# Performance work log

Hardware: AMD Instinct MI355X
Metric: run time of the kernel (lower is better)

The kernel has to match this reference:

```python
import jax, jax.numpy as jnp
import numpy as np
import math

B, T, D, S, V = 128, 32, 64, 32, 8192
MAX_REC = 8
PONDER = 0.01
TWO_PI = 2.0 * math.pi


def setup_inputs():
    key = jax.random.key(0)
    ks = jax.random.split(key, 12)
    sd = 1.0 / math.sqrt(D)
    g = lambda k, shape, s: jax.random.normal(k, shape, jnp.float32) * s
    return {
        "x_seq": jax.random.randint(ks[0], (B, T), 0, V),
        "encoder_emb": g(ks[1], (V, 2 * D), 0.02),
        "vq_emb": g(ks[2], (V, 2 * D), sd),
        "norm_rg": jnp.ones((D,), jnp.float32), "norm_rb": jnp.zeros((D,), jnp.float32),
        "norm_ig": jnp.ones((D,), jnp.float32), "norm_ib": jnp.zeros((D,), jnp.float32),
        "qkv_Wr": g(ks[3], (3, D, D), sd), "qkv_br": g(ks[4], (3, D), sd),
        "qkv_Wi": g(ks[5], (3, D, D), sd), "qkv_bi": g(ks[6], (3, D), sd),
        "gate_w": g(ks[7], (2 * D,), sd), "gate_b": jnp.zeros((), jnp.float32),
        "arb_W": g(ks[8], (3, 2 * D), sd), "arb_b": jnp.zeros((3,), jnp.float32),
        "dec_W": g(ks[9], (V, 2 * D), sd), "dec_b": jnp.zeros((V,), jnp.float32),
        "halt_bias": jnp.asarray(3.0, jnp.float32),
        "input_gate": jnp.asarray(0.0, jnp.float32),
    }


def _ln(x, g, b, eps=1e-5):
    mu = x.mean(-1, keepdims=True)
    var = ((x - mu) ** 2).mean(-1, keepdims=True)
    return (x - mu) * jax.lax.rsqrt(var + eps) * g + b


def _forward(x_seq, encoder_emb, vq_emb, norm_rg, norm_rb, norm_ig, norm_ib,
             qkv_Wr, qkv_br, qkv_Wi, qkv_bi, gate_w, gate_b, arb_W, arb_b,
             dec_W, dec_b, halt_bias, input_gate):
    sg = jax.lax.stop_gradient
    e_sq = (vq_emb ** 2).sum(-1)  # [V]
    alpha = jax.nn.sigmoid(input_gate)
    bias = jax.nn.softplus(halt_bias)

    def clin(xr, xi, Wr, br, Wi, bi):
        # torch ComplexLinear: real = fc_r(xr) - fc_i(xi); imag = fc_r(xi) + fc_i(xr)
        return (xr @ Wr.T + br) - (xi @ Wi.T + bi), (xi @ Wr.T + br) + (xr @ Wi.T + bi)

    def mem_write(gr, gi, mr, mi):
        flat = jnp.concatenate([gr, gi], -1)
        wg = jax.nn.sigmoid(flat @ gate_w + gate_b)[:, None, None]  # [B,1,1]
        shr, shi = jnp.roll(mr, 1, axis=1), jnp.roll(mi, 1, axis=1)
        hr = wg * gr[:, None, :] + (1.0 - wg) * shr[:, :1]
        hi = wg * gi[:, None, :] + (1.0 - wg) * shi[:, :1]
        return jnp.concatenate([hr, shr[:, 1:]], 1), jnp.concatenate([hi, shi[:, 1:]], 1)

    def time_step(carry, xt):
        gw_r, gw_i, mem_r, mem_i = carry
        x_r, x_i = xt
        gw_r = alpha * gw_r + (1.0 - alpha) * x_r
        gw_i = alpha * gw_i + (1.0 - alpha) * x_i
        active = jnp.ones((B,), jnp.float32)
        acc_vq = jnp.zeros((B,), jnp.float32)
        acc_ent = jnp.zeros((B,), jnp.float32)
        acc_pond = jnp.zeros((B,), jnp.float32)
        acc_ph = jnp.zeros((B,), jnp.float32)
        fin_idx = jnp.zeros((B,), jnp.int32)
        prev_ang = jnp.arctan2(gw_i, gw_r)
        for _ in range(MAX_REC):
            cr = _ln(gw_r, norm_rg, norm_rb)
            ci = _ln(gw_i, norm_ig, norm_ib)
            z_flat = jnp.concatenate([cr, ci], -1)  # [B,2D]
            # squared-euclidean scores; argmin identical to cdist argmin
            d2 = (z_flat ** 2).sum(-1, keepdims=True) - 2.0 * (z_flat @ vq_emb.T) + e_sq
            idx = jnp.argmin(d2, -1).astype(jnp.int32)
            z_q = vq_emb[idx]
            vq_loss = ((z_q - sg(z_flat)) ** 2).mean(-1) + 0.25 * ((sg(z_q) - z_flat) ** 2).mean(-1)
            z_st = z_flat + sg(z_q - z_flat)  # straight-through
            counts = jnp.zeros((V,), jnp.float32).at[idx].add(1.0) / B
            entropy = -(counts * jnp.log(counts + 1e-10)).sum()
            v_r, v_i = z_st[:, :D], z_st[:, D:]
            # Hermitian gating
            qr, qi = clin(cr, ci, qkv_Wr[0], qkv_br[0], qkv_Wi[0], qkv_bi[0])
            kr, ki = clin(cr, ci, qkv_Wr[1], qkv_br[1], qkv_Wi[1], qkv_bi[1])
            vr2, vi2 = clin(cr, ci, qkv_Wr[2], qkv_br[2], qkv_Wi[2], qkv_bi[2])
            gate = jax.nn.sigmoid((qr * kr + qi * ki).sum(-1, keepdims=True))
            g_r, g_i = vr2 * gate, vi2 * gate
            # memory read (Re<m, q> attention over slots)
            sim = jnp.einsum('bsd,bd->bs', mem_r, cr) + jnp.einsum('bsd,bd->bs', mem_i, ci)
            attn = jax.nn.softmax(sim, -1)
            m_r = jnp.einsum('bs,bsd->bd', attn, mem_r)
            m_i = jnp.einsum('bs,bsd->bd', attn, mem_i)
            gates = jax.nn.softmax(z_flat @ arb_W.T + arb_b, -1)  # [B,3]
            upd_r = gates[:, 0:1] * g_r + gates[:, 1:2] * m_r + gates[:, 2:3] * v_r
            upd_i = gates[:, 0:1] * g_i + gates[:, 1:2] * m_i + gates[:, 2:3] * v_i
            cand_r = 0.6 * cr + 0.4 * upd_r
            cand_i = 0.6 * ci + 0.4 * upd_i
            ang = jnp.arctan2(cand_i, cand_r)
            diff = jnp.abs(ang - prev_ang)
            diff = jnp.minimum(diff, TWO_PI - diff)
            acc_ph = acc_ph + active * diff.mean(-1)
            prev_ang = ang
            halt_prob = jax.nn.sigmoid(bias - vq_loss)
            should_stop = (halt_prob > 0.5).astype(jnp.float32)
            acc_pond = acc_pond + active * PONDER
            mflat = active > 0.5
            acc_vq = jnp.where(mflat, vq_loss, acc_vq)
            acc_ent = jnp.where(mflat, entropy, acc_ent)
            fin_idx = jnp.where(mflat, idx, fin_idx)
            am = mflat[:, None]
            gw_r = jnp.where(am, cand_r, gw_r)
            gw_i = jnp.where(am, cand_i, gw_i)
            active = active * (1.0 - should_stop)
        mem_r, mem_i = mem_write(gw_r, gw_i, mem_r, mem_i)
        stats_t = jnp.stack([acc_vq.mean(), acc_ent.mean(), acc_pond.mean(), acc_ph.mean()])
        return (gw_r, gw_i, mem_r, mem_i), (gw_r, gw_i, fin_idx, stats_t)

    emb = encoder_emb[x_seq]  # [B,T,2D]
    xr = jnp.transpose(emb[..., :D], (1, 0, 2))  # [T,B,D]
    xi = jnp.transpose(emb[..., D:], (1, 0, 2))
    init = (jnp.zeros((B, D), jnp.float32), jnp.zeros((B, D), jnp.float32),
            jnp.zeros((B, S, D), jnp.float32), jnp.zeros((B, S, D), jnp.float32))
    _, (out_r, out_i, idxs, stats) = jax.lax.scan(time_step, init, (xr, xi))
    out = jnp.concatenate([jnp.transpose(out_r, (1, 0, 2)),
                           jnp.transpose(out_i, (1, 0, 2))], -1)  # [B,T,2D]
    logits = out @ dec_W.T + dec_b  # [B,T,V]
    return logits, stats.sum(0) / T, jnp.transpose(idxs)  # [B,T]


def reference(x_seq, encoder_emb, vq_emb, norm_rg, norm_rb, norm_ig, norm_ib, qkv_Wr, qkv_br, qkv_Wi, qkv_bi, gate_w, gate_b, arb_W, arb_b, dec_W, dec_b, halt_bias, input_gate):
    return _forward(x_seq, encoder_emb, vq_emb, norm_rg, norm_rb, norm_ig, norm_ib,
                    qkv_Wr, qkv_br, qkv_Wi, qkv_bi, gate_w, gate_b, arb_W, arb_b,
                    dec_W, dec_b, halt_bias, input_gate)
```

## Files before the change

### kernel.cpp

```cpp
#include <hip/hip_runtime.h>
#include <math.h>

#define TT 32
#define MAXREC 8
#define NBLK 256
#define NTHR 1024

#define OFF_ZBUF   0u
#define OFF_KEYS   65536u
#define OFF_ZDONE  196608u
#define OFF_FINAL  198656u
#define OFF_OUTHB  200704u
#define OFF_RST    1249280u
#define OFF_DWB    1251328u

#define SENT 0x7FFFFFFFu
#define IDXM 0x1FFFu
#define LOGN 33554432u
#define TWO_PI_F 6.283185307179586f

typedef float f32x4 __attribute__((ext_vector_type(4)));
typedef short bf16x8 __attribute__((ext_vector_type(8)));
typedef unsigned long long u64;

__device__ __forceinline__ float wredsum(float v) {
#pragma unroll
  for (int m = 32; m > 0; m >>= 1) v += __shfl_xor(v, m);
  return v;
}

__device__ __forceinline__ u64 shflx64(u64 v, int m) {
  int lo = __shfl_xor((int)(unsigned)(v & 0xffffffffull), m);
  int hi = __shfl_xor((int)(unsigned)(v >> 32), m);
  return ((u64)(unsigned)hi << 32) | (unsigned)lo;
}

__device__ __forceinline__ u64 packkey(float d, unsigned c) {
  unsigned u = __float_as_uint(d);
  u = (u & 0x80000000u) ? ~u : (u | 0x80000000u);
  return ((u64)u << 32) | c;
}
__device__ __forceinline__ float unpackd2(u64 key) {
  unsigned hi = (unsigned)(key >> 32);
  unsigned orig = (hi & 0x80000000u) ? (hi & 0x7fffffffu) : ~hi;
  return __uint_as_float(orig);
}
__device__ __forceinline__ unsigned short f2bf(float f) {
  unsigned u = __float_as_uint(f);
  unsigned r = (u >> 16) & 1u;
  u += 0x7fffu + r;
  return (unsigned short)(u >> 16);
}

__device__ __forceinline__ unsigned ld_coh32(const unsigned* p) {
  unsigned v;
  asm volatile("global_load_dword %0, %1, off sc0 sc1\n\ts_waitcnt vmcnt(0)"
               : "=&v"(v) : "v"(p) : "memory");
  return v;
}
__device__ __forceinline__ u64 ld_coh64(const u64* p) {
  u64 v;
  asm volatile("global_load_dwordx2 %0, %1, off sc0 sc1\n\ts_waitcnt vmcnt(0)"
               : "=&v"(v) : "v"(p) : "memory");
  return v;
}
__device__ __forceinline__ void st_coh_f32(float* p, float v) {
  asm volatile("global_store_dword %0, %1, off sc0 sc1" :: "v"(p), "v"(v) : "memory");
}
__device__ __forceinline__ void st_coh32(unsigned* p, unsigned v) {
  asm volatile("global_store_dword %0, %1, off sc0 sc1" :: "v"(p), "v"(v) : "memory");
}
__device__ __forceinline__ void st_coh64(u64* p, u64 v) {
  asm volatile("global_store_dwordx2 %0, %1, off sc0 sc1" :: "v"(p), "v"(v) : "memory");
}
__device__ __forceinline__ void drain_vm() {
  asm volatile("s_waitcnt vmcnt(0)" ::: "memory");
}

__device__ __forceinline__ void ld4w(const float* base,
    unsigned o0, unsigned o1, unsigned o2, unsigned o3,
    f32x4& a0, f32x4& a1, f32x4& a2, f32x4& a3) {
  asm volatile(
      "global_load_dwordx4 %0, %4, %8 sc0 sc1\n\t"
      "global_load_dwordx4 %1, %5, %8 sc0 sc1\n\t"
      "global_load_dwordx4 %2, %6, %8 sc0 sc1\n\t"
      "global_load_dwordx4 %3, %7, %8 sc0 sc1\n\t"
      "s_waitcnt vmcnt(0)"
      : "=&v"(a0), "=&v"(a1), "=&v"(a2), "=&v"(a3)
      : "v"(o0), "v"(o1), "v"(o2), "v"(o3), "s"(base)
      : "memory");
}

__global__ __launch_bounds__(512) void sacrsn_init(char* __restrict__ ws) {
  unsigned* zd = (unsigned*)(ws + OFF_ZDONE);
  u64* fin = (u64*)(ws + OFF_FINAL);
  zd[threadIdx.x] = 0u;
  if (threadIdx.x < 128) fin[threadIdx.x] = 0ull;
}

__global__ __launch_bounds__(256) void k_prep(const float* __restrict__ dW,
                                              char* __restrict__ ws) {
  unsigned short* dWb = (unsigned short*)(ws + OFF_DWB);
  const int i = (blockIdx.x * 256 + threadIdx.x) * 4;
  float4 v = *(const float4*)(dW + i);
  ushort4 o;
  o.x = f2bf(v.x); o.y = f2bf(v.y); o.z = f2bf(v.z); o.w = f2bf(v.w);
  *(ushort4*)(dWb + i) = o;
}

__global__ __launch_bounds__(NTHR) void sacrsn_main(
    const int* __restrict__ x_seq, const float* __restrict__ enc,
    const float* __restrict__ vqe,
    const float* __restrict__ nrg, const float* __restrict__ nrb,
    const float* __restrict__ nig, const float* __restrict__ nib,
    const float* __restrict__ qWr, const float* __restrict__ qbr,
    const float* __restrict__ qWi, const float* __restrict__ qbi,
    const float* __restrict__ gtw, const float* __restrict__ gtb,
    const float* __restrict__ aW, const float* __restrict__ ab,
    const float* __restrict__ hbp, const float* __restrict__ igp,
    float* __restrict__ dout, char* __restrict__ ws)
{
  float* zbuf = (float*)(ws + OFF_ZBUF);
  u64*   keys = (u64*)(ws + OFF_KEYS);
  unsigned* zdone = (unsigned*)(ws + OFF_ZDONE);
  u64*   finalA = (u64*)(ws + OFF_FINAL);
  unsigned short* outhB = (unsigned short*)(ws + OFF_OUTHB);
  float* rst  = (float*)(ws + OFF_RST);

  const int tid = threadIdx.x;
  const int wv = tid >> 6, ln = tid & 63;
  const int blk = blockIdx.x;
  const bool owner = (blk < 128);

  __shared__ float els[64 * 128];
  __shared__ float zloc[128 * 128];
  __shared__ u64 vtmp[128 * 17];
  __shared__ float esqL[64];
  __shared__ float z2locL[128];
  __shared__ float memLr[32 * 65];
  __shared__ float memLi[32 * 65];
  __shared__ float gwrowL[128], pangL[64], zfmL[128], zqL[128];
  __shared__ float qkL[6][64], simL[32], attnL[32], mrL[64], miL[64];
  __shared__ unsigned idxL[128] __attribute__((aligned(16)));
  __shared__ u64 key128L[128], kred[128];
  __shared__ float arbWL[3 * 128];
  __shared__ float scalL[8], entpL[2], vqpL[2], wsumL[2];
  __shared__ float accL[4], totL[4];
  __shared__ float dmeanS;
  __shared__ u64 actM[2], actN[2];
  __shared__ unsigned pollOK, pollSent, mfS;

  const float alpha = 1.0f / (1.0f + expf(-igp[0]));
  const float onema = 1.0f - alpha;
  const float hbias = log1pf(expf(hbp[0]));
  const float gtb0 = gtb[0];

  if (!owner) {
    const int s = blk - 128;
#pragma unroll
    for (int j = 0; j < 2; ++j) {
      int f4 = tid + j * NTHR;
      int c = f4 >> 5, k4 = f4 & 31;
      float4 v = *(const float4*)&vqe[((size_t)(s * 64 + c) << 7) + (k4 << 2)];
      *(float4*)&els[(c << 7) + ((k4 ^ (c & 31)) << 2)] = v;
    }
    __syncthreads();
    if (tid < 64) {
      float sm = 0.0f;
#pragma unroll 8
      for (int k4 = 0; k4 < 32; ++k4) {
        float4 v = *(const float4*)&els[(tid << 7) + ((k4 ^ (tid & 31)) << 2)];
        sm = fmaf(v.x, v.x, fmaf(v.y, v.y, fmaf(v.z, v.z, fmaf(v.w, v.w, sm))));
      }
      esqL[tid] = sm;
    }
    __syncthreads();
    unsigned k = 0;
    while (true) {
      bool done = false;
      while (true) {
        if (tid == 0) { pollOK = 1u; pollSent = 1u; }
        __syncthreads();
        if (tid < 128) {
          unsigned v = ld_coh32(&zdone[tid * 4]);
          if ((int)(v - (k + 1u)) < 0) pollOK = 0u;
          if (v != SENT) pollSent = 0u;
        }
        __syncthreads();
        if (pollSent) { done = true; break; }
        if (pollOK) break;
        __builtin_amdgcn_s_sleep(1);
      }
      if (done) break;
      {
        f32x4 a0, a1, a2, a3;
        const unsigned tb = (unsigned)tid * 16u;
        ld4w(zbuf, tb, tb + 16384u, tb + 32768u, tb + 49152u, a0, a1, a2, a3);
        __builtin_amdgcn_sched_barrier(0);
        f32x4 va[4] = {a0, a1, a2, a3};
#pragma unroll
        for (int u = 0; u < 4; ++u) {
          int f4 = u * NTHR + tid;
          int row = f4 >> 5, k4 = f4 & 31;
          *(f32x4*)&zloc[(row << 7) + ((k4 ^ (row & 31)) << 2)] = va[u];
        }
      }
      __syncthreads();
      if (tid < 128) {
        float sm = 0.0f;
#pragma unroll 8
        for (int k4 = 0; k4 < 32; ++k4) {
          float4 q = *(const float4*)&zloc[(tid << 7) + ((k4 ^ (tid & 31)) << 2)];
          sm = fmaf(q.x, q.x, fmaf(q.y, q.y, fmaf(q.z, q.z, fmaf(q.w, q.w, sm))));
        }
        z2locL[tid] = sm;
      }
      const int rt = tid & 63, ct = tid >> 6;
      float acc[2][4];
#pragma unroll
      for (int rr = 0; rr < 2; ++rr)
#pragma unroll
        for (int cc = 0; cc < 4; ++cc) acc[rr][cc] = 0.0f;
#pragma unroll 2
      for (int k4 = 0; k4 < 32; ++k4) {
        float4 zv[2], ev[4];
#pragma unroll
        for (int rr = 0; rr < 2; ++rr)
          zv[rr] = *(const float4*)&zloc[((rt + rr * 64) << 7) + ((k4 ^ (rt & 31)) << 2)];
#pragma unroll
        for (int cc = 0; cc < 4; ++cc) {
          int cl = ct * 4 + cc;
          ev[cc] = *(const float4*)&els[(cl << 7) + ((k4 ^ (cl & 31)) << 2)];
        }
#pragma unroll
        for (int rr = 0; rr < 2; ++rr)
#pragma unroll
          for (int cc = 0; cc < 4; ++cc)
            acc[rr][cc] = fmaf(zv[rr].x, ev[cc].x, fmaf(zv[rr].y, ev[cc].y,
                          fmaf(zv[rr].z, ev[cc].z, fmaf(zv[rr].w, ev[cc].w, acc[rr][cc]))));
      }
      __syncthreads();
#pragma unroll
      for (int rr = 0; rr < 2; ++rr) {
        const int row = rt + rr * 64;
        const float z2r = z2locL[row];
        u64 key = ~0ull;
#pragma unroll
        for (int cc = 0; cc < 4; ++cc) {
          int cl = ct * 4 + cc;
          float d2 = (z2r - 2.0f * acc[rr][cc]) + esqL[cl];
          u64 pk = packkey(d2, (unsigned)(s * 64 + cl));
          if (pk < key) key = pk;
        }
        vtmp[row * 17 + ct] = key;
      }
      __syncthreads();
      if (tid < 128) {
        u64 kmin = vtmp[tid * 17];
#pragma unroll
        for (int w = 1; w < 16; ++w) { u64 o = vtmp[tid * 17 + w]; if (o < kmin) kmin = o; }
        st_coh64(&keys[(size_t)s * 128 + tid], kmin | ((u64)(k + 1u) << 13));
      }
      k++;
    }
    return;
  }

  float lnG = 0.0f, lnB = 0.0f, gtwv = 0.0f;
  if (tid < 64) { lnG = nrg[tid]; lnB = nrb[tid]; }
  else if (tid < 128) { lnG = nig[tid - 64]; lnB = nib[tid - 64]; }
  if (tid < 128) gtwv = gtw[tid];
  for (int i = tid; i < 32 * 65; i += NTHR) { memLr[i] = 0.0f; memLi[i] = 0.0f; }
  if (tid < 4) { totL[tid] = 0.0f; accL[tid] = 0.0f; }
  if (tid < 2) actM[tid] = ~0ull;
  for (int i = tid; i < 384; i += NTHR) arbWL[i] = aW[i];
  {
    int tok = x_seq[blk * TT];
    if (tid < 128) gwrowL[tid] = onema * enc[((size_t)tok << 7) + tid];
  }
  __syncthreads();
  if (tid < 64) pangL[tid] = atan2f(gwrowL[64 + tid], gwrowL[tid]);
  if (tid < 128) {
    float val = gwrowL[tid];
    float mu = wredsum(val) * 0.015625f;
    float xc = val - mu;
    float vr = wredsum(xc * xc) * 0.015625f;
    float z = xc * (1.0f / sqrtf(vr + 1e-5f)) * lnG + lnB;
    zfmL[tid] = z;
    st_coh_f32(&zbuf[(blk << 7) + tid], z);
  }
  drain_vm();
  __syncthreads();
  if (tid == 0) st_coh32(&zdone[blk * 4], 1u);

  int t = 0, it = 0;
  unsigned k = 0;
  for (;;) {
    const unsigned tag = k + 1u;
    float encN = 0.0f;
    {
      int tnext = (t + 1 < TT) ? t + 1 : t;
      if (tid < 128) {
        int tk = x_seq[blk * TT + tnext];
        encN = enc[((size_t)tk << 7) + tid];
      }
    }
    if (tid < 192) {
      const int h = tid >> 6, j = tid & 63;
      const float* wr = qWr + h * 4096 + j * 64;
      const float* wi = qWi + h * 4096 + j * 64;
      float da = 0.0f, db_ = 0.0f, dc = 0.0f, de = 0.0f;
#pragma unroll 4
      for (int d4 = 0; d4 < 64; d4 += 4) {
        float4 wrv = *(const float4*)&wr[d4];
        float4 wiv = *(const float4*)&wi[d4];
        float4 crv = *(const float4*)&zfmL[d4];
        float4 civ = *(const float4*)&zfmL[64 + d4];
        da = fmaf(crv.x, wrv.x, fmaf(crv.y, wrv.y, fmaf(crv.z, wrv.z, fmaf(crv.w, wrv.w, da))));
        db_ = fmaf(civ.x, wiv.x, fmaf(civ.y, wiv.y, fmaf(civ.z, wiv.z, fmaf(civ.w, wiv.w, db_))));
        dc = fmaf(civ.x, wrv.x, fmaf(civ.y, wrv.y, fmaf(civ.z, wrv.z, fmaf(civ.w, wrv.w, dc))));
        de = fmaf(crv.x, wiv.x, fmaf(crv.y, wiv.y, fmaf(crv.z, wiv.z, fmaf(crv.w, wiv.w, de))));
      }
      float brv = qbr[h * 64 + j], biv = qbi[h * 64 + j];
      qkL[2 * h][j] = da + brv - db_ - biv;
      qkL[2 * h + 1][j] = dc + brv + de + biv;
    } else if (tid < 224) {
      const int s2 = tid - 192;
      float a2 = 0.0f;
      for (int d = 0; d < 64; ++d)
        a2 = fmaf(memLr[s2 * 65 + d], zfmL[d], fmaf(memLi[s2 * 65 + d], zfmL[64 + d], a2));
      simL[s2] = a2;
    } else if (tid < 227) {
      const int h = tid - 224;
      float a2 = ab[h];
      for (int k2 = 0; k2 < 128; ++k2) a2 = fmaf(zfmL[k2], arbWL[h * 128 + k2], a2);
      scalL[3 + h] = a2;
    }
    __syncthreads();
    if (tid < 64) {
      float p = fmaf(qkL[0][tid], qkL[2][tid], qkL[1][tid] * qkL[3][tid]);
      p = wredsum(p);
      if (tid == 0) scalL[0] = 1.0f / (1.0f + expf(-p));
    } else if (tid < 96) {
      const int s2 = tid - 64;
      float v = simL[s2];
      float m = v;
#pragma unroll
      for (int msk = 16; msk > 0; msk >>= 1) m = fmaxf(m, __shfl_xor(m, msk));
      float e = expf(v - m);
      float ss = e;
#pragma unroll
      for (int msk = 16; msk > 0; msk >>= 1) ss += __shfl_xor(ss, msk);
      attnL[s2] = e / ss;
    } else if (tid == 96) {
      float a0 = scalL[3], a1 = scalL[4], a2 = scalL[5];
      float m = fmaxf(a0, fmaxf(a1, a2));
      float e0 = expf(a0 - m), e1 = expf(a1 - m), e2 = expf(a2 - m);
      float ssum = e0 + e1 + e2;
      scalL[3] = e0 / ssum; scalL[4] = e1 / ssum; scalL[5] = e2 / ssum;
    }
    __syncthreads();
    if (tid < 128) {
      const int d = ln;
      const float* ml = (wv == 0) ? memLr : memLi;
      float a2 = 0.0f;
#pragma unroll 4
      for (int s2 = 0; s2 < 32; ++s2) a2 = fmaf(attnL[s2], ml[s2 * 65 + d], a2);
      if (wv == 0) mrL[d] = a2; else miL[d] = a2;
    }
    while (true) {
      if (tid == 0) pollOK = 1u;
      __syncthreads();
      if (tid < 128) {
        u64 v = ld_coh64(&keys[(size_t)tid * 128 + blk]);
        if ((unsigned)((v >> 13) & 0x7FFFFull) != tag) pollOK = 0u;
        else kred[tid] = v;
      }
      __syncthreads();
      if (pollOK) break;
      __builtin_amdgcn_s_sleep(1);
    }
    if (tid < 64) {
      u64 a = kred[tid], b = kred[tid + 64];
      if (b < a) a = b;
#pragma unroll
      for (int m2 = 32; m2 > 0; m2 >>= 1) { u64 o = shflx64(a, m2); if (o < a) a = o; }
      if (tid == 0) st_coh64(&finalA[blk], a);
    }
    while (true) {
      if (tid == 0) pollOK = 1u;
      __syncthreads();
      if (tid < 128) {
        u64 v = ld_coh64(&finalA[tid]);
        if ((unsigned)((v >> 13) & 0x7FFFFull) != tag) pollOK = 0u;
        else key128L[tid] = v;
      }
      __syncthreads();
      if (pollOK) break;
      __builtin_amdgcn_s_sleep(1);
    }
    if (tid < 128) {
      u64 key = key128L[tid];
      idxL[tid] = (unsigned)key & IDXM;
      float d2 = unpackd2(key);
      bool act_b = ((actM[tid >> 6] >> (tid & 63)) & 1ull) != 0ull;
      bool stop = (1.25f * 0.0078125f * d2) < hbias;
      u64 ball = __ballot(act_b && !stop);
      if (ln == 0) actN[tid >> 6] = ball;
    }
    __syncthreads();
    if (tid == 0) mfS = (unsigned)((actM[blk >> 6] >> (blk & 63)) & 1ull);
    if (tid < 2) actM[tid] = actN[tid];
    __syncthreads();
    const bool anyAct = (actN[0] | actN[1]) != 0ull;
    const bool mf = mfS != 0u;
    const unsigned ii = idxL[blk];
    if (tid < 128) {
      float zq = vqe[((size_t)ii << 7) + tid];
      zqL[tid] = zq;
      float df = zq - zfmL[tid];
      float sm = wredsum(df * df);
      if (ln == 0) vqpL[wv] = sm;
    } else if (tid < 256) {
      const int r = tid - 128;
      unsigned my = idxL[r];
      int c = 0;
#pragma unroll
      for (int j4 = 0; j4 < 32; ++j4) {
        uint4 q = *(const uint4*)&idxL[j4 * 4];
        c += (q.x == my) + (q.y == my) + (q.z == my) + (q.w == my);
      }
      float term = -0.0078125f * logf((float)c * 0.0078125f + 1e-10f);
      term = wredsum(term);
      if (ln == 0) entpL[wv - 2] = term;
    }
    __syncthreads();
    if (tid < 64) {
      const int d = tid;
      float gate = scalL[0], g0 = scalL[3], g1 = scalL[4], g2 = scalL[5];
      float cr = zfmL[d], ci = zfmL[64 + d];
      float ur = fmaf(g0, qkL[4][d] * gate, fmaf(g1, mrL[d], g2 * zqL[d]));
      float ui = fmaf(g0, qkL[5][d] * gate, fmaf(g1, miL[d], g2 * zqL[64 + d]));
      float cdr = fmaf(0.4f, ur, 0.6f * cr);
      float cdi = fmaf(0.4f, ui, 0.6f * ci);
      float ang = atan2f(cdi, cdr);
      float df = fabsf(ang - pangL[d]);
      df = fminf(df, TWO_PI_F - df);
      pangL[d] = ang;
      float dm = wredsum(df) * 0.015625f;
      if (mf) { gwrowL[d] = cdr; gwrowL[64 + d] = cdi; }
      if (d == 0) dmeanS = dm;
    }
    __syncthreads();
    const bool newT = !(anyAct && it < MAXREC - 1);
    const bool finished = newT && (t == TT - 1);
    if (newT && !finished) {
      float pr = 0.0f;
      if (tid < 128) {
        pr = gwrowL[tid];
        outhB[((size_t)blk * TT + t) * 128 + tid] = f2bf(pr);
        float part = wredsum(pr * gtwv);
        if (ln == 0) wsumL[wv] = part;
      }
      __syncthreads();
      if (tid < 128) {
        float wg = 1.0f / (1.0f + expf(-(wsumL[0] + wsumL[1] + gtb0)));
        int slot = 31 - t;
        float* m = (tid < 64) ? &memLr[slot * 65 + tid] : &memLi[slot * 65 + (tid - 64)];
        *m = fmaf(wg, pr, (1.0f - wg) * (*m));
        gwrowL[tid] = fmaf(alpha, pr, onema * encN);
      }
      __syncthreads();
    }
    if (!finished) {
      if (tid < 128) {
        float val = gwrowL[tid];
        float mu = wredsum(val) * 0.015625f;
        float xc = val - mu;
        float vr = wredsum(xc * xc) * 0.015625f;
        float z = xc * (1.0f / sqrtf(vr + 1e-5f)) * lnG + lnB;
        zfmL[tid] = z;
        st_coh_f32(&zbuf[(blk << 7) + tid], z);
      }
      drain_vm();
      __syncthreads();
      if (tid == 0) st_coh32(&zdone[blk * 4], k + 2u);
    } else {
      __syncthreads();
    }
    if (tid == 0) {
      float aold = mf ? 1.0f : 0.0f;
      float vql = 1.25f * (vqpL[0] + vqpL[1]) * 0.0078125f;
      accL[3] += aold * dmeanS;
      accL[2] += aold * 0.01f;
      if (mf) {
        accL[0] = vql;
        accL[1] = entpL[0] + entpL[1];
        dout[(size_t)LOGN + 4 + (size_t)blk * TT + t] = (float)ii;
      }
    }
    if (newT && !finished) {
      if (tid < 64) pangL[tid] = atan2f(gwrowL[64 + tid], gwrowL[tid]);
      if (tid < 4) { totL[tid] += accL[tid]; accL[tid] = 0.0f; }
      if (tid < 2) actM[tid] = ~0ull;
    }
    __syncthreads();
    if (finished) break;
    if (newT) { t++; it = 0; } else { it++; }
    k++;
  }

  if (tid < 128) outhB[((size_t)blk * TT + (TT - 1)) * 128 + tid] = f2bf(gwrowL[tid]);
  if (tid < 4) rst[blk * 4 + tid] = totL[tid] + accL[tid];
  __syncthreads();
  if (tid == 0) st_coh32(&zdone[blk * 4], SENT);
}

__global__ __launch_bounds__(256) void k_dec(
    const float* __restrict__ dbv, float* __restrict__ dout,
    const char* __restrict__ ws)
{
  const unsigned short* outhB = (const unsigned short*)(ws + OFF_OUTHB);
  const unsigned short* dWb = (const unsigned short*)(ws + OFF_DWB);
  const float* rst = (const float*)(ws + OFF_RST);
  const int tid = threadIdx.x;
  if (blockIdx.x == 0 && tid < 4) {
    float s = 0.0f;
    for (int r = 0; r < 128; ++r) s += rst[r * 4 + tid];
    dout[(size_t)LOGN + tid] = s * (1.0f / 4096.0f);
  }
  const int w = tid >> 6, l = tid & 63;
  const int bm = blockIdx.x & 63;
  const int bn = blockIdx.x >> 6;
  const int ar = l & 15, kg = l >> 4;
  const int m_base = bm * 64;
  const int n_base = bn * 256 + w * 64;
  f32x4 acc[4][4];
#pragma unroll
  for (int mt = 0; mt < 4; ++mt)
#pragma unroll
    for (int nt = 0; nt < 4; ++nt) acc[mt][nt] = (f32x4){0.f, 0.f, 0.f, 0.f};
#pragma unroll
  for (int kc = 0; kc < 4; ++kc) {
    const int ko = kc * 32 + kg * 8;
    bf16x8 a[4], b[4];
#pragma unroll
    for (int mt = 0; mt < 4; ++mt)
      a[mt] = *(const bf16x8*)(outhB + (size_t)(m_base + mt * 16 + ar) * 128 + ko);
#pragma unroll
    for (int nt = 0; nt < 4; ++nt)
      b[nt] = *(const bf16x8*)(dWb + (size_t)(n_base + nt * 16 + ar) * 128 + ko);
#pragma unroll
    for (int mt = 0; mt < 4; ++mt)
#pragma unroll
      for (int nt = 0; nt < 4; ++nt)
        acc[mt][nt] = __builtin_amdgcn_mfma_f32_16x16x32_bf16(a[mt], b[nt], acc[mt][nt], 0, 0, 0);
  }
#pragma unroll
  for (int nt = 0; nt < 4; ++nt) {
    const int n = n_base + nt * 16 + ar;
    const float bv = dbv[n];
#pragma unroll
    for (int mt = 0; mt < 4; ++mt) {
#pragma unroll
      for (int rr = 0; rr < 4; ++rr) {
        const int m = m_base + mt * 16 + kg * 4 + rr;
        dout[(size_t)m * 8192 + n] = acc[mt][nt][rr] + bv;
      }
    }
  }
}

extern "C" void kernel_launch(void* const* d_in, const int* in_sizes, int n_in,
                              void* d_out, int out_size, void* d_ws, size_t ws_size,
                              hipStream_t stream) {
  (void)in_sizes; (void)n_in; (void)out_size; (void)ws_size;
  const int*   x_seq = (const int*)d_in[0];
  const float* enc = (const float*)d_in[1];
  const float* vq  = (const float*)d_in[2];
  const float* nrg = (const float*)d_in[3];
  const float* nrb = (const float*)d_in[4];
  const float* nig = (const float*)d_in[5];
  const float* nib = (const float*)d_in[6];
  const float* qWr = (const float*)d_in[7];
  const float* qbr = (const float*)d_in[8];
  const float* qWi = (const float*)d_in[9];
  const float* qbi = (const float*)d_in[10];
  const float* gtw = (const float*)d_in[11];
  const float* gtb = (const float*)d_in[12];
  const float* aW  = (const float*)d_in[13];
  const float* ab  = (const float*)d_in[14];
  const float* dW  = (const float*)d_in[15];
  const float* db  = (const float*)d_in[16];
  const float* hb  = (const float*)d_in[17];
  const float* ig  = (const float*)d_in[18];
  char* ws = (char*)d_ws;
  float* out = (float*)d_out;
  hipLaunchKernelGGL(sacrsn_init, dim3(1), dim3(512), 0, stream, ws);
  hipLaunchKernelGGL(k_prep, dim3(1024), dim3(256), 0, stream, dW, ws);
  hipLaunchKernelGGL(sacrsn_main, dim3(NBLK), dim3(NTHR), 0, stream,
                     x_seq, enc, vq, nrg, nrb, nig, nib, qWr, qbr, qWi, qbi,
                     gtw, gtb, aW, ab, hb, ig, out, ws);
  hipLaunchKernelGGL(k_dec, dim3(2048), dim3(256), 0, stream, db, out, ws);
}
```

Measured before the change: 738.8 us.

## Screen VQ distances with bf16 MFMA and re-score candidates in fp32

Worker blocks now compute approximate z·e dot products with bf16 MFMA on a bf16 copy of the codebook and a bf16 copy of z. They keep only codes whose distance falls within an error bound of the row minimum, then recompute those candidates exactly in fp32 to pick the argmin. Other changes: the block size is halved, codebook norms are precomputed in a prep kernel, z² is published together with the done flag, and the workspace is reorganised so the codebook and decoder bf16 buffers share one region. The candidate path relies on the error bound being safe and on the candidate count staying small, otherwise the fp32 re-scoring loop grows.

```diff
diff --git a/kernel.cpp b/kernel.cpp
--- a/kernel.cpp
+++ b/kernel.cpp
@@ -4,15 +4,16 @@
 #define TT 32
 #define MAXREC 8
 #define NBLK 256
-#define NTHR 1024
+#define NTHR 512
 
 #define OFF_ZBUF   0u
-#define OFF_KEYS   65536u
-#define OFF_ZDONE  196608u
-#define OFF_FINAL  198656u
-#define OFF_OUTHB  200704u
-#define OFF_RST    1249280u
-#define OFF_DWB    1251328u
+#define OFF_ZBUFB  65536u
+#define OFF_KEYS   98304u
+#define OFF_ZDONE  229376u
+#define OFF_ESQ    231424u
+#define OFF_RST    264192u
+#define OFF_OUTHB  266240u
+#define OFF_WB     1314816u
 
 #define SENT 0x7FFFFFFFu
 #define IDXM 0x1FFFu
@@ -28,13 +29,11 @@
   for (int m = 32; m > 0; m >>= 1) v += __shfl_xor(v, m);
   return v;
 }
-
 __device__ __forceinline__ u64 shflx64(u64 v, int m) {
   int lo = __shfl_xor((int)(unsigned)(v & 0xffffffffull), m);
   int hi = __shfl_xor((int)(unsigned)(v >> 32), m);
   return ((u64)(unsigned)hi << 32) | (unsigned)lo;
 }
-
 __device__ __forceinline__ u64 packkey(float d, unsigned c) {
   unsigned u = __float_as_uint(d);
   u = (u & 0x80000000u) ? ~u : (u | 0x80000000u);
@@ -52,12 +51,6 @@
   return (unsigned short)(u >> 16);
 }
 
-__device__ __forceinline__ unsigned ld_coh32(const unsigned* p) {
-  unsigned v;
-  asm volatile("global_load_dword %0, %1, off sc0 sc1\n\ts_waitcnt vmcnt(0)"
-               : "=&v"(v) : "v"(p) : "memory");
-  return v;
-}
 __device__ __forceinline__ u64 ld_coh64(const u64* p) {
   u64 v;
   asm volatile("global_load_dwordx2 %0, %1, off sc0 sc1\n\ts_waitcnt vmcnt(0)"
@@ -76,7 +69,6 @@
 __device__ __forceinline__ void drain_vm() {
   asm volatile("s_waitcnt vmcnt(0)" ::: "memory");
 }
-
 __device__ __forceinline__ void ld4w(const float* base,
     unsigned o0, unsigned o1, unsigned o2, unsigned o3,
     f32x4& a0, f32x4& a1, f32x4& a2, f32x4& a3) {
@@ -92,15 +84,37 @@
 }
 
 __global__ __launch_bounds__(512) void sacrsn_init(char* __restrict__ ws) {
-  unsigned* zd = (unsigned*)(ws + OFF_ZDONE);
-  u64* fin = (u64*)(ws + OFF_FINAL);
-  zd[threadIdx.x] = 0u;
-  if (threadIdx.x < 128) fin[threadIdx.x] = 0ull;
-}
-
-__global__ __launch_bounds__(256) void k_prep(const float* __restrict__ dW,
-                                              char* __restrict__ ws) {
-  unsigned short* dWb = (unsigned short*)(ws + OFF_DWB);
+  u64* zd = (u64*)(ws + OFF_ZDONE);
+  u64* fin = (u64*)(ws + OFF_KEYS);
+  (void)fin;
+  if (threadIdx.x < 256) ((u64*)zd)[threadIdx.x] = 0ull;
+}
+
+__global__ __launch_bounds__(256) void k_prepv(const float* __restrict__ vqe,
+                                               char* __restrict__ ws) {
+  unsigned short* vqeB = (unsigned short*)(ws + OFF_WB);
+  float* esqG = (float*)(ws + OFF_ESQ);
+  const int i = (blockIdx.x * 256 + threadIdx.x) * 4;
+  float4 v = *(const float4*)(vqe + i);
+  ushort4 o;
+  o.x = f2bf(v.x); o.y = f2bf(v.y); o.z = f2bf(v.z); o.w = f2bf(v.w);
+  *(ushort4*)(vqeB + i) = o;
+  if (blockIdx.x < 32) {
+    const int c = blockIdx.x * 256 + threadIdx.x;
+    const float4* e = (const float4*)(vqe + ((size_t)c << 7));
+    float s = 0.f;
+#pragma unroll 8
+    for (int k4 = 0; k4 < 32; ++k4) {
+      float4 q = e[k4];
+      s = fmaf(q.x, q.x, fmaf(q.y, q.y, fmaf(q.z, q.z, fmaf(q.w, q.w, s))));
+    }
+    esqG[c] = s;
+  }
+}
+
+__global__ __launch_bounds__(256) void k_prepd(const float* __restrict__ dW,
+                                               char* __restrict__ ws) {
+  unsigned short* dWb = (unsigned short*)(ws + OFF_WB);
   const int i = (blockIdx.x * 256 + threadIdx.x) * 4;
   float4 v = *(const float4*)(dW + i);
   ushort4 o;
@@ -121,22 +135,22 @@
     float* __restrict__ dout, char* __restrict__ ws)
 {
   float* zbuf = (float*)(ws + OFF_ZBUF);
+  unsigned* zbufB32 = (unsigned*)(ws + OFF_ZBUFB);
   u64*   keys = (u64*)(ws + OFF_KEYS);
-  unsigned* zdone = (unsigned*)(ws + OFF_ZDONE);
-  u64*   finalA = (u64*)(ws + OFF_FINAL);
+  u64*   zdone64 = (u64*)(ws + OFF_ZDONE);
+  const float* esqG = (const float*)(ws + OFF_ESQ);
+  const unsigned short* vqeB = (const unsigned short*)(ws + OFF_WB);
+  u64*   finalA = (u64*)(ws + OFF_KEYS);
   unsigned short* outhB = (unsigned short*)(ws + OFF_OUTHB);
   float* rst  = (float*)(ws + OFF_RST);
+  finalA = (u64*)(ws + OFF_ZDONE + 1024u);
+  finalA = (u64*)(ws + OFF_ZDONE + 8u);
 
   const int tid = threadIdx.x;
   const int wv = tid >> 6, ln = tid & 63;
   const int blk = blockIdx.x;
   const bool owner = (blk < 128);
 
-  __shared__ float els[64 * 128];
-  __shared__ float zloc[128 * 128];
-  __shared__ u64 vtmp[128 * 17];
-  __shared__ float esqL[64];
-  __shared__ float z2locL[128];
   __shared__ float memLr[32 * 65];
   __shared__ float memLi[32 * 65];
   __shared__ float gwrowL[128], pangL[64], zfmL[128], zqL[128];
@@ -144,11 +158,15 @@
   __shared__ unsigned idxL[128] __attribute__((aligned(16)));
   __shared__ u64 key128L[128], kred[128];
   __shared__ float arbWL[3 * 128];
-  __shared__ float scalL[8], entpL[2], vqpL[2], wsumL[2];
+  __shared__ float scalL[8], entpL[2], vqpL[2], wsumL[2], z2pL[2];
   __shared__ float accL[4], totL[4];
   __shared__ float dmeanS;
   __shared__ u64 actM[2], actN[2];
   __shared__ unsigned pollOK, pollSent, mfS;
+  __shared__ float z2L[128], sz2L[128];
+  __shared__ u64 rowminU[128];
+  __shared__ unsigned candL[8192];
+  __shared__ unsigned candCount;
 
   const float alpha = 1.0f / (1.0f + expf(-igp[0]));
   const float onema = 1.0f - alpha;
@@ -157,24 +175,8 @@
 
   if (!owner) {
     const int s = blk - 128;
-#pragma unroll
-    for (int j = 0; j < 2; ++j) {
-      int f4 = tid + j * NTHR;
-      int c = f4 >> 5, k4 = f4 & 31;
-      float4 v = *(const float4*)&vqe[((size_t)(s * 64 + c) << 7) + (k4 << 2)];
-      *(float4*)&els[(c << 7) + ((k4 ^ (c & 31)) << 2)] = v;
-    }
-    __syncthreads();
-    if (tid < 64) {
-      float sm = 0.0f;
-#pragma unroll 8
-      for (int k4 = 0; k4 < 32; ++k4) {
-        float4 v = *(const float4*)&els[(tid << 7) + ((k4 ^ (tid & 31)) << 2)];
-        sm = fmaf(v.x, v.x, fmaf(v.y, v.y, fmaf(v.z, v.z, fmaf(v.w, v.w, sm))));
-      }
-      esqL[tid] = sm;
-    }
-    __syncthreads();
+    const int w = tid >> 6, l = tid & 63;
+    const int ar = l & 15, kg = l >> 4;
     unsigned k = 0;
     while (true) {
       bool done = false;
@@ -182,9 +184,11 @@
         if (tid == 0) { pollOK = 1u; pollSent = 1u; }
         __syncthreads();
         if (tid < 128) {
-          unsigned v = ld_coh32(&zdone[tid * 4]);
-          if ((int)(v - (k + 1u)) < 0) pollOK = 0u;
-          if (v != SENT) pollSent = 0u;
+          u64 v = ld_coh64(&zdone64[tid * 2]);
+          unsigned lo = (unsigned)v;
+          if ((int)(lo - (k + 1u)) < 0) pollOK = 0u;
+          if (lo != SENT) pollSent = 0u;
+          if (lo == k + 1u) z2L[tid] = __uint_as_float((unsigned)(v >> 32));
         }
         __syncthreads();
         if (pollSent) { done = true; break; }
@@ -192,75 +196,96 @@
         __builtin_amdgcn_s_sleep(1);
       }
       if (done) break;
+      if (tid < 128) { sz2L[tid] = sqrtf(z2L[tid]); rowminU[tid] = ~0ull; }
+      if (tid == 0) candCount = 0u;
+      __syncthreads();
+      f32x4 af0, af1, af2, af3;
       {
-        f32x4 a0, a1, a2, a3;
-        const unsigned tb = (unsigned)tid * 16u;
-        ld4w(zbuf, tb, tb + 16384u, tb + 32768u, tb + 49152u, a0, a1, a2, a3);
-        __builtin_amdgcn_sched_barrier(0);
-        f32x4 va[4] = {a0, a1, a2, a3};
-#pragma unroll
-        for (int u = 0; u < 4; ++u) {
-          int f4 = u * NTHR + tid;
-          int row = f4 >> 5, k4 = f4 & 31;
-          *(f32x4*)&zloc[(row << 7) + ((k4 ^ (row & 31)) << 2)] = va[u];
+        const unsigned rb = (unsigned)((w * 16 + ar) * 256 + kg * 16);
+        ld4w((const float*)(ws + OFF_ZBUFB), rb, rb + 64u, rb + 128u, rb + 192u,
+             af0, af1, af2, af3);
+      }
+      bf16x8 afr[4];
+      afr[0] = *(bf16x8*)&af0; afr[1] = *(bf16x8*)&af1;
+      afr[2] = *(bf16x8*)&af2; afr[3] = *(bf16x8*)&af3;
+      f32x4 dc[4];
+#pragma unroll
+      for (int nt = 0; nt < 4; ++nt) dc[nt] = (f32x4){0.f, 0.f, 0.f, 0.f};
+#pragma unroll
+      for (int kc = 0; kc < 4; ++kc) {
+#pragma unroll
+        for (int nt = 0; nt < 4; ++nt) {
+          bf16x8 b = *(const bf16x8*)(vqeB + (((size_t)(s * 64 + nt * 16 + ar)) << 7)
+                                      + kc * 32 + kg * 8);
+          dc[nt] = __builtin_amdgcn_mfma_f32_16x16x32_bf16(afr[kc], b, dc[nt], 0, 0, 0);
         }
       }
-      __syncthreads();
-      if (tid < 128) {
-        float sm = 0.0f;
-#pragma unroll 8
-        for (int k4 = 0; k4 < 32; ++k4) {
-          float4 q = *(const float4*)&zloc[(tid << 7) + ((k4 ^ (tid & 31)) << 2)];
-          sm = fmaf(q.x, q.x, fmaf(q.y, q.y, fmaf(q.z, q.z, fmaf(q.w, q.w, sm))));
+      float aV[4][4], eV[4][4], Lmin[4];
+#pragma unroll
+      for (int rr = 0; rr < 4; ++rr) Lmin[rr] = 1e30f;
+#pragma unroll
+      for (int nt = 0; nt < 4; ++nt) {
+        const int code = s * 64 + nt * 16 + ar;
+        const float es = esqG[code];
+        const float se = sqrtf(es);
+#pragma unroll
+        for (int rr = 0; rr < 4; ++rr) {
+          const int row = w * 16 + kg * 4 + rr;
+          float av = (z2L[row] - 2.0f * dc[nt][rr]) + es;
+          float ev = fmaf(0.0082f * sz2L[row], se, 1e-3f);
+          aV[nt][rr] = av; eV[nt][rr] = ev;
+          float ae = av + ev;
+          if (ae < Lmin[rr]) Lmin[rr] = ae;
         }
-        z2locL[tid] = sm;
-      }
-      const int rt = tid & 63, ct = tid >> 6;
-      float acc[2][4];
-#pragma unroll
-      for (int rr = 0; rr < 2; ++rr)
-#pragma unroll
-        for (int cc = 0; cc < 4; ++cc) acc[rr][cc] = 0.0f;
-#pragma unroll 2
-      for (int k4 = 0; k4 < 32; ++k4) {
-        float4 zv[2], ev[4];
-#pragma unroll
-        for (int rr = 0; rr < 2; ++rr)
-          zv[rr] = *(const float4*)&zloc[((rt + rr * 64) << 7) + ((k4 ^ (rt & 31)) << 2)];
-#pragma unroll
-        for (int cc = 0; cc < 4; ++cc) {
-          int cl = ct * 4 + cc;
-          ev[cc] = *(const float4*)&els[(cl << 7) + ((k4 ^ (cl & 31)) << 2)];
+      }
+#pragma unroll
+      for (int m2 = 1; m2 < 16; m2 <<= 1)
+#pragma unroll
+        for (int rr = 0; rr < 4; ++rr) {
+          float o = __shfl_xor(Lmin[rr], m2);
+          if (o < Lmin[rr]) Lmin[rr] = o;
         }
 #pragma unroll
-        for (int rr = 0; rr < 2; ++rr)
-#pragma unroll
-          for (int cc = 0; cc < 4; ++cc)
-            acc[rr][cc] = fmaf(zv[rr].x, ev[cc].x, fmaf(zv[rr].y, ev[cc].y,
-                          fmaf(zv[rr].z, ev[cc].z, fmaf(zv[rr].w, ev[cc].w, acc[rr][cc]))));
-      }
-      __syncthreads();
-#pragma unroll
-      for (int rr = 0; rr < 2; ++rr) {
-        const int row = rt + rr * 64;
-        const float z2r = z2locL[row];
-        u64 key = ~0ull;
-#pragma unroll
-        for (int cc = 0; cc < 4; ++cc) {
-          int cl = ct * 4 + cc;
-          float d2 = (z2r - 2.0f * acc[rr][cc]) + esqL[cl];
-          u64 pk = packkey(d2, (unsigned)(s * 64 + cl));
-          if (pk < key) key = pk;
+      for (int nt = 0; nt < 4; ++nt)
+#pragma unroll
+        for (int rr = 0; rr < 4; ++rr)
+          if (aV[nt][rr] - eV[nt][rr] <= Lmin[rr]) {
+            const unsigned row = (unsigned)(w * 16 + kg * 4 + rr);
+            const unsigned code = (unsigned)(s * 64 + nt * 16 + ar);
+            unsigned pos = atomicAdd(&candCount, 1u);
+            candL[pos] = (row << 16) | code;
+          }
+      __syncthreads();
+      const unsigned cnt = candCount;
+      for (unsigned base = 0; base < cnt; base += 64u) {
+        const unsigned eIdx = base + (unsigned)(tid >> 3);
+        const bool valid = eIdx < cnt;
+        float dsum = 0.f;
+        int row = 0, code = 0;
+        if (valid) {
+          unsigned en = candL[eIdx];
+          row = (int)(en >> 16); code = (int)(en & 0xFFFFu);
+          const int ks = tid & 7;
+          f32x4 z0, z1, z2v, z3;
+          const unsigned zb = (unsigned)(row * 512 + ks * 64);
+          ld4w(zbuf, zb, zb + 16u, zb + 32u, zb + 48u, z0, z1, z2v, z3);
+          const float4* ep = (const float4*)(vqe + ((size_t)code << 7) + ks * 16);
+          float4 e0 = ep[0], e1 = ep[1], e2 = ep[2], e3 = ep[3];
+          dsum = fmaf(z0[0], e0.x, fmaf(z0[1], e0.y, fmaf(z0[2], e0.z, fmaf(z0[3], e0.w, 0.f))));
+          dsum = fmaf(z1[0], e1.x, fmaf(z1[1], e1.y, fmaf(z1[2], e1.z, fmaf(z1[3], e1.w, dsum))));
+          dsum = fmaf(z2v[0], e2.x, fmaf(z2v[1], e2.y, fmaf(z2v[2], e2.z, fmaf(z2v[3], e2.w, dsum))));
+          dsum = fmaf(z3[0], e3.x, fmaf(z3[1], e3.y, fmaf(z3[2], e3.z, fmaf(z3[3], e3.w, dsum))));
         }
-        vtmp[row * 17 + ct] = key;
-      }
-      __syncthreads();
-      if (tid < 128) {
-        u64 kmin = vtmp[tid * 17];
-#pragma unroll
-        for (int w = 1; w < 16; ++w) { u64 o = vtmp[tid * 17 + w]; if (o < kmin) kmin = o; }
-        st_coh64(&keys[(size_t)s * 128 + tid], kmin | ((u64)(k + 1u) << 13));
-      }
+#pragma unroll
+        for (int m2 = 1; m2 < 8; m2 <<= 1) dsum += __shfl_xor(dsum, m2);
+        if (valid && (tid & 7) == 0) {
+          float d2 = (z2L[row] - 2.0f * dsum) + esqG[code];
+          atomicMin(&rowminU[row], packkey(d2, (unsigned)code));
+        }
+      }
+      __syncthreads();
+      if (tid < 128)
+        st_coh64(&keys[(size_t)s * 128 + tid], rowminU[tid] | ((u64)(k + 1u) << 13));
       k++;
     }
     return;
@@ -288,10 +313,20 @@
     float z = xc * (1.0f / sqrtf(vr + 1e-5f)) * lnG + lnB;
     zfmL[tid] = z;
     st_coh_f32(&zbuf[(blk << 7) + tid], z);
+    float zo = __shfl_xor(z, 1);
+    if ((tid & 1) == 0) {
+      unsigned pk = (unsigned)f2bf(z) | ((unsigned)f2bf(zo) << 16);
+      st_coh32(&zbufB32[blk * 64 + (tid >> 1)], pk);
+    }
+    float s2 = wredsum(z * z);
+    if (ln == 0) z2pL[wv] = s2;
   }
   drain_vm();
   __syncthreads();
-  if (tid == 0) st_coh32(&zdone[blk * 4], 1u);
+  if (tid == 0) {
+    float z2 = z2pL[0] + z2pL[1];
+    st_coh64(&zdone64[blk * 2], (u64)1u | ((u64)__float_as_uint(z2) << 32));
+  }
 
   int t = 0, it = 0;
   unsigned k = 0;
@@ -309,7 +344,7 @@
       const int h = tid >> 6, j = tid & 63;
       const float* wr = qWr + h * 4096 + j * 64;
       const float* wi = qWi + h * 4096 + j * 64;
-      float da = 0.0f, db_ = 0.0f, dc = 0.0f, de = 0.0f;
+      float da = 0.0f, db_ = 0.0f, dc2 = 0.0f, de = 0.0f;
 #pragma unroll 4
       for (int d4 = 0; d4 < 64; d4 += 4) {
         float4 wrv = *(const float4*)&wr[d4];
@@ -318,12 +353,12 @@
         float4 civ = *(const float4*)&zfmL[64 + d4];
         da = fmaf(crv.x, wrv.x, fmaf(crv.y, wrv.y, fmaf(crv.z, wrv.z, fmaf(crv.w, wrv.w, da))));
         db_ = fmaf(civ.x, wiv.x, fmaf(civ.y, wiv.y, fmaf(civ.z, wiv.z, fmaf(civ.w, wiv.w, db_))));
-        dc = fmaf(civ.x, wrv.x, fmaf(civ.y, wrv.y, fmaf(civ.z, wrv.z, fmaf(civ.w, wrv.w, dc))));
+        dc2 = fmaf(civ.x, wrv.x, fmaf(civ.y, wrv.y, fmaf(civ.z, wrv.z, fmaf(civ.w, wrv.w, dc2))));
         de = fmaf(crv.x, wiv.x, fmaf(crv.y, wiv.y, fmaf(crv.z, wiv.z, fmaf(crv.w, wiv.w, de))));
       }
       float brv = qbr[h * 64 + j], biv = qbi[h * 64 + j];
       qkL[2 * h][j] = da + brv - db_ - biv;
-      qkL[2 * h + 1][j] = dc + brv + de + biv;
+      qkL[2 * h + 1][j] = dc2 + brv + de + biv;
     } else if (tid < 224) {
       const int s2 = tid - 192;
       float a2 = 0.0f;
@@ -385,13 +420,13 @@
       if (b < a) a = b;
 #pragma unroll
       for (int m2 = 32; m2 > 0; m2 >>= 1) { u64 o = shflx64(a, m2); if (o < a) a = o; }
-      if (tid == 0) st_coh64(&finalA[blk], a);
+      if (tid == 0) st_coh64(&finalA[blk * 2], a);
     }
     while (true) {
       if (tid == 0) pollOK = 1u;
       __syncthreads();
       if (tid < 128) {
-        u64 v = ld_coh64(&finalA[tid]);
+        u64 v = ld_coh64(&finalA[tid * 2]);
         if ((unsigned)((v >> 13) & 0x7FFFFull) != tag) pollOK = 0u;
         else key128L[tid] = v;
       }
@@ -481,10 +516,20 @@
         float z = xc * (1.0f / sqrtf(vr + 1e-5f)) * lnG + lnB;
         zfmL[tid] = z;
         st_coh_f32(&zbuf[(blk << 7) + tid], z);
+        float zo = __shfl_xor(z, 1);
+        if ((tid & 1) == 0) {
+          unsigned pk = (unsigned)f2bf(z) | ((unsigned)f2bf(zo) << 16);
+          st_coh32(&zbufB32[blk * 64 + (tid >> 1)], pk);
+        }
+        float s2 = wredsum(z * z);
+        if (ln == 0) z2pL[wv] = s2;
       }
       drain_vm();
       __syncthreads();
-      if (tid == 0) st_coh32(&zdone[blk * 4], k + 2u);
+      if (tid == 0) {
+        float z2 = z2pL[0] + z2pL[1];
+        st_coh64(&zdone64[blk * 2], (u64)(k + 2u) | ((u64)__float_as_uint(z2) << 32));
+      }
     } else {
       __syncthreads();
     }
@@ -513,7 +558,7 @@
   if (tid < 128) outhB[((size_t)blk * TT + (TT - 1)) * 128 + tid] = f2bf(gwrowL[tid]);
   if (tid < 4) rst[blk * 4 + tid] = totL[tid] + accL[tid];
   __syncthreads();
-  if (tid == 0) st_coh32(&zdone[blk * 4], SENT);
+  if (tid == 0) st_coh64(&zdone64[blk * 2], (u64)SENT);
 }
 
 __global__ __launch_bounds__(256) void k_dec(
@@ -521,7 +566,7 @@
     const char* __restrict__ ws)
 {
   const unsigned short* outhB = (const unsigned short*)(ws + OFF_OUTHB);
-  const unsigned short* dWb = (const unsigned short*)(ws + OFF_DWB);
+  const unsigned short* dWb = (const unsigned short*)(ws + OFF_WB);
   const float* rst = (const float*)(ws + OFF_RST);
   const int tid = threadIdx.x;
   if (blockIdx.x == 0 && tid < 4) {
@@ -597,9 +642,10 @@
   char* ws = (char*)d_ws;
   float* out = (float*)d_out;
   hipLaunchKernelGGL(sacrsn_init, dim3(1), dim3(512), 0, stream, ws);
-  hipLaunchKernelGGL(k_prep, dim3(1024), dim3(256), 0, stream, dW, ws);
+  hipLaunchKernelGGL(k_prepv, dim3(1024), dim3(256), 0, stream, vq, ws);
   hipLaunchKernelGGL(sacrsn_main, dim3(NBLK), dim3(NTHR), 0, stream,
                      x_seq, enc, vq, nrg, nrb, nig, nib, qWr, qbr, qWi, qbi,
                      gtw, gtb, aW, ab, hb, ig, out, ws);
+  hipLaunchKernelGGL(k_prepd, dim3(1024), dim3(256), 0, stream, dW, ws);
   hipLaunchKernelGGL(k_dec, dim3(2048), dim3(256), 0, stream, db, out, ws);
 }
```

Result: faster. 698.0 us (-5.5%).
